# Kernel optimization log

Hardware: AMD Instinct MI355X
Metric: run time of the kernel (lower is better)

## Reference

```python
import jax, jax.numpy as jnp
import numpy as np

KH = KW = 3
STRIDE = 1
PAD = 1
DIL = 1


def _bilinear_sample(img, py, px):
    Hin, Win = img.shape[-2], img.shape[-1]
    y0 = jnp.floor(py)
    x0 = jnp.floor(px)
    y0i = y0.astype(jnp.int32)
    x0i = x0.astype(jnp.int32)
    wy = py - y0
    wx = px - x0

    def get(yi, xi):
        valid = (yi >= 0) & (yi < Hin) & (xi >= 0) & (xi < Win)
        yc = jnp.clip(yi, 0, Hin - 1)
        xc = jnp.clip(xi, 0, Win - 1)
        v = img[:, yc, xc]  # [C, K, H, W]
        return v * valid[None].astype(img.dtype)

    v00 = get(y0i, x0i)
    v01 = get(y0i, x0i + 1)
    v10 = get(y0i + 1, x0i)
    v11 = get(y0i + 1, x0i + 1)
    return (v00 * (1 - wy) * (1 - wx) + v01 * (1 - wy) * wx
            + v10 * wy * (1 - wx) + v11 * wy * wx)  # [C, K, H, W]


def _deform_conv(input, offset, mask, weight, bias):
    B, C, H, W = input.shape
    outH = (H + 2 * PAD - DIL * (KH - 1) - 1) // STRIDE + 1
    outW = (W + 2 * PAD - DIL * (KW - 1) - 1) // STRIDE + 1
    K = KH * KW
    # NOTE: DepthOffset in the original source overwrites its computed
    # depth-guided offsets with zeros and detaches them, so the effective
    # sampling offset is just `offset` (standard modulated deform conv, DCNv2).
    off = offset.reshape(B, K, 2, outH, outW)
    off_y = off[:, :, 0]  # [B, K, outH, outW]
    off_x = off[:, :, 1]
    ky = (jnp.arange(K) // KW) * DIL  # kernel-tap row offsets
    kx = (jnp.arange(K) % KW) * DIL
    ys = jnp.arange(outH) * STRIDE - PAD
    xs = jnp.arange(outW) * STRIDE - PAD
    base_y = (ky[:, None, None] + ys[None, :, None]).astype(input.dtype)  # [K, outH, 1]
    base_x = (kx[:, None, None] + xs[None, None, :]).astype(input.dtype)  # [K, 1, outW]
    py = base_y[None] + off_y  # [B, K, outH, outW]
    px = base_x[None] + off_x
    cols = jax.vmap(_bilinear_sample)(input, py, px)  # [B, C, K, outH, outW]
    cols = cols * mask[:, None]  # modulate by mask [B, 1, K, outH, outW]
    out = jnp.einsum('bckhw,ock->bohw', cols, weight.reshape(weight.shape[0], C, K))
    return out + bias[None, :, None, None]


def setup_inputs() -> dict:
    key = jax.random.key(0)
    ks = jax.random.split(key, 6)
    B, C, H, W = 4, 64, 128, 128
    O = 64
    fan_in = C * KH * KW
    bound = 1.0 / np.sqrt(fan_in)
    return {
        'input': jax.random.normal(ks[0], (B, C, H, W), dtype=jnp.float32),
        'depth': jax.random.uniform(ks[1], (B, 1, H, W), dtype=jnp.float32),
        'offset': jax.random.normal(ks[2], (B, 18, H, W), dtype=jnp.float32),
        'mask': jax.random.uniform(ks[3], (B, 9, H, W), dtype=jnp.float32),
        'weight': jax.random.uniform(ks[4], (O, C, KH, KW), dtype=jnp.float32,
                                     minval=-bound, maxval=bound),
        'bias': jax.random.uniform(ks[5], (O,), dtype=jnp.float32,
                                   minval=-bound, maxval=bound),
    }


def reference(input, depth, offset, mask, weight, bias):
    # depth-guided offsets are computed then zeroed+detached in the original
    # module, so depth does not influence the output.
    return _deform_conv(input, offset, mask, weight, bias)
```

## Files before the change

kernel.cpp:

```cpp
#include <hip/hip_runtime.h>


typedef __attribute__((ext_vector_type(8))) short bf16x8;
typedef __attribute__((ext_vector_type(4))) float f32x4;
typedef __attribute__((ext_vector_type(4))) unsigned int u32x4;

#define HH 128
#define WW 128
#define CC 64
#define OO 64
#define HW (128 * 128)

__device__ __forceinline__ unsigned f32_to_bf16_rne(float f) {
    unsigned u = __float_as_uint(f);
    return (u + 0x7FFFu + ((u >> 16) & 1u)) >> 16;
}

__global__ __launch_bounds__(256)
void prep_nhwc(const float* __restrict__ input,
               unsigned short* __restrict__ nhwc)
{
    __shared__ unsigned tile[64][33];
    const int tid = threadIdx.x;
    const int blk = blockIdx.x;
    const int b  = blk >> 9;
    const int y  = (blk >> 2) & 127;
    const int xbase = (blk & 3) * 32;
    #pragma unroll
    for (int it = 0; it < 8; ++it) {
        int flat = it * 256 + tid;
        int c = flat >> 5, x = flat & 31;
        float v = input[((b * 64 + c) * 128 + y) * 128 + xbase + x];
        tile[c][x] = f32_to_bf16_rne(v);
    }
    __syncthreads();
    {
        int x = tid >> 3, cg = tid & 7;
        unsigned r0 = tile[cg * 8 + 0][x], r1 = tile[cg * 8 + 1][x];
        unsigned r2 = tile[cg * 8 + 2][x], r3 = tile[cg * 8 + 3][x];
        unsigned r4 = tile[cg * 8 + 4][x], r5 = tile[cg * 8 + 5][x];
        unsigned r6 = tile[cg * 8 + 6][x], r7 = tile[cg * 8 + 7][x];
        u32x4 pk;
        pk[0] = r0 | (r1 << 16); pk[1] = r2 | (r3 << 16);
        pk[2] = r4 | (r5 << 16); pk[3] = r6 | (r7 << 16);
        *(u32x4*)(nhwc + ((size_t)((b * 128 + y) * 128 + xbase + x)) * 64 + cg * 8) = pk;
    }
}

__global__ __launch_bounds__(256)
void prep_w(const float* __restrict__ weight,
            unsigned short* __restrict__ wT2)
{
    const int d  = blockIdx.x * 256 + threadIdx.x;
    const int o  = d & 63;
    const int k8 = d >> 6;
    const int kt = k8 >> 3;
    const int c8 = k8 & 7;
    u32x4 pk;
    #pragma unroll
    for (int jj = 0; jj < 4; ++jj) {
        unsigned lo = f32_to_bf16_rne(weight[o * 576 + (c8 * 8 + 2 * jj)     * 9 + kt]);
        unsigned hi = f32_to_bf16_rne(weight[o * 576 + (c8 * 8 + 2 * jj + 1) * 9 + kt]);
        pk[jj] = lo | (hi << 16);
    }
    *(u32x4*)(wT2 + (size_t)d * 8) = pk;
}

__global__ __launch_bounds__(512)
void ddc_main(const unsigned short* __restrict__ nhwc,
              const unsigned short* __restrict__ wT2,
              const float* __restrict__ offset,
              const float* __restrict__ mask,
              const float* __restrict__ bias,
              float* __restrict__ out)
{
    __shared__ u32x4 wbuf[2560];

    const int blk  = blockIdx.x;
    const int b    = blk >> 7;
    const int h    = blk & 127;
    const int tid  = threadIdx.x;
    const int wave = tid >> 6;
    const int lane = tid & 63;
    const int l15  = lane & 15;
    const int kq   = lane >> 4;
    const int wpix = wave * 16 + l15;

    f32x4 acc[4];
    #pragma unroll
    for (int mt = 0; mt < 4; ++mt) acc[mt] = (f32x4){0.f, 0.f, 0.f, 0.f};

    const unsigned short* nb = nhwc + (size_t)b * HW * CC;
    const u32x4* wsrc = (const u32x4*)wT2;

    auto do_tap = [&](int kt, int ktl) {
        const float oy = offset[((b * 18 + 2 * kt)     * 128 + h) * 128 + wpix];
        const float ox = offset[((b * 18 + 2 * kt + 1) * 128 + h) * 128 + wpix];
        const float m  = mask  [((b * 9  + kt)         * 128 + h) * 128 + wpix];
        const float py = (float)(h - 1 + kt / 3) + oy;
        const float px = (float)(wpix - 1 + kt % 3) + ox;
        const float y0f = floorf(py), x0f = floorf(px);
        const int y0 = (int)y0f, x0 = (int)x0f;
        const float wy = py - y0f, wx = px - x0f;
        const int y1 = y0 + 1, x1 = x0 + 1;
        const bool vy0 = (y0 >= 0) & (y0 < HH);
        const bool vy1 = (y1 >= 0) & (y1 < HH);
        const bool vx0 = (x0 >= 0) & (x0 < WW);
        const bool vx1 = (x1 >= 0) & (x1 < WW);
        const int y0c = min(max(y0, 0), HH - 1), y1c = min(max(y1, 0), HH - 1);
        const int x0c = min(max(x0, 0), WW - 1), x1c = min(max(x1, 0), WW - 1);
        const float wy1 = 1.f - wy, wx1 = 1.f - wx;
        const float c00 = (vy0 && vx0) ? wy1 * wx1 * m : 0.f;
        const float c01 = (vy0 && vx1) ? wy1 * wx  * m : 0.f;
        const float c10 = (vy1 && vx0) ? wy  * wx1 * m : 0.f;
        const float c11 = (vy1 && vx1) ? wy  * wx  * m : 0.f;

        #pragma unroll
        for (int ks = 0; ks < 2; ++ks) {
            const int c0 = ks * 32 + kq * 8;

            const u32x4 w00 = *(const u32x4*)(nb + (y0c * WW + x0c) * CC + c0);
            const u32x4 w01 = *(const u32x4*)(nb + (y0c * WW + x1c) * CC + c0);
            const u32x4 w10 = *(const u32x4*)(nb + (y1c * WW + x0c) * CC + c0);
            const u32x4 w11 = *(const u32x4*)(nb + (y1c * WW + x1c) * CC + c0);

            u32x4 pk;
            #pragma unroll
            for (int j = 0; j < 4; ++j) {
                const float a0 = __uint_as_float(w00[j] << 16);
                const float a1 = __uint_as_float(w00[j] & 0xFFFF0000u);
                const float b0 = __uint_as_float(w01[j] << 16);
                const float b1 = __uint_as_float(w01[j] & 0xFFFF0000u);
                const float d0 = __uint_as_float(w10[j] << 16);
                const float d1 = __uint_as_float(w10[j] & 0xFFFF0000u);
                const float e0 = __uint_as_float(w11[j] << 16);
                const float e1 = __uint_as_float(w11[j] & 0xFFFF0000u);
                const float s0 = c00 * a0 + c01 * b0 + c10 * d0 + c11 * e0;
                const float s1 = c00 * a1 + c01 * b1 + c10 * d1 + c11 * e1;
                pk[j] = f32_to_bf16_rne(s0) | (f32_to_bf16_rne(s1) << 16);
            }
            const bf16x8 bfrag = __builtin_bit_cast(bf16x8, pk);

            #pragma unroll
            for (int mt = 0; mt < 4; ++mt) {
                const bf16x8 afrag = __builtin_bit_cast(bf16x8,
                    wbuf[(ktl * 8 + ks * 4 + kq) * 64 + mt * 16 + l15]);
                acc[mt] = __builtin_amdgcn_mfma_f32_16x16x32_bf16(afrag, bfrag, acc[mt], 0, 0, 0);
            }
        }
    };

    #pragma unroll
    for (int i = 0; i < 5; ++i) wbuf[i * 512 + tid] = wsrc[i * 512 + tid];
    __syncthreads();
    #pragma unroll
    for (int kt = 0; kt < 5; ++kt) do_tap(kt, kt);
    __syncthreads();

    #pragma unroll
    for (int i = 0; i < 4; ++i) wbuf[i * 512 + tid] = wsrc[2560 + i * 512 + tid];
    __syncthreads();
    #pragma unroll
    for (int kt = 5; kt < 9; ++kt) do_tap(kt, kt - 5);

    #pragma unroll
    for (int mt = 0; mt < 4; ++mt) {
        const f32x4 bv = *(const f32x4*)(bias + mt * 16 + kq * 4);
        #pragma unroll
        for (int r = 0; r < 4; ++r) {
            const int o = mt * 16 + kq * 4 + r;
            out[((b * 64 + o) * 128 + h) * 128 + wpix] = acc[mt][r] + bv[r];
        }
    }
}

extern "C" void kernel_launch(void* const* d_in, const int* in_sizes, int n_in,
                              void* d_out, int out_size, void* d_ws, size_t ws_size,
                              hipStream_t stream)
{
    const float* input  = (const float*)d_in[0];
    const float* offset = (const float*)d_in[2];
    const float* mask   = (const float*)d_in[3];
    const float* weight = (const float*)d_in[4];
    const float* bias   = (const float*)d_in[5];
    float* out = (float*)d_out;

    unsigned short* nhwc = (unsigned short*)d_ws;
    unsigned short* wT2  = nhwc + (size_t)4 * HW * CC;

    prep_nhwc<<<dim3(2048), dim3(256), 0, stream>>>(input, nhwc);
    prep_w<<<dim3(18), dim3(256), 0, stream>>>(weight, wT2);
    ddc_main<<<dim3(512), dim3(512), 0, stream>>>(nhwc, wT2, offset, mask, bias, out);
}
```

Baseline: 119.0 us.

## Stage an 8-row input window in LDS and double-buffer per-tap weights

The main kernel now loads an 8-row NHWC window around the output row into LDS, with an XOR swizzle on channel groups, so bilinear gathers read from LDS. Samples whose rows fall outside the window still read global memory. Weights are streamed one tap at a time through a double buffer instead of two large batches. The block index is remapped across batches, and the two prep kernels are merged into one launch. LDS use rises to roughly 144KB per block, which limits occupancy to one block per CU and adds a full 8-row window load before any compute starts.

Result: faster. 114.8 us (-3.5%).

```diff
diff --git a/kernel.cpp b/kernel.cpp
--- a/kernel.cpp
+++ b/kernel.cpp
@@ -17,12 +17,32 @@
 }
 
 __global__ __launch_bounds__(256)
-void prep_nhwc(const float* __restrict__ input,
-               unsigned short* __restrict__ nhwc)
+void prep_fused9(const float* __restrict__ input,
+                 unsigned short* __restrict__ nhwc,
+                 const float* __restrict__ weight,
+                 unsigned short* __restrict__ wT2)
 {
     __shared__ unsigned tile[64][33];
     const int tid = threadIdx.x;
     const int blk = blockIdx.x;
+
+    if (blk >= 2048) {
+        const int d  = (blk - 2048) * 256 + tid;
+        const int o  = d & 63;
+        const int k8 = d >> 6;
+        const int kt = k8 >> 3;
+        const int c8 = k8 & 7;
+        u32x4 pk;
+        #pragma unroll
+        for (int jj = 0; jj < 4; ++jj) {
+            unsigned lo = f32_to_bf16_rne(weight[o * 576 + (c8 * 8 + 2 * jj)     * 9 + kt]);
+            unsigned hi = f32_to_bf16_rne(weight[o * 576 + (c8 * 8 + 2 * jj + 1) * 9 + kt]);
+            pk[jj] = lo | (hi << 16);
+        }
+        *(u32x4*)(wT2 + (size_t)d * 8) = pk;
+        return;
+    }
+
     const int b  = blk >> 9;
     const int y  = (blk >> 2) & 127;
     const int xbase = (blk & 3) * 32;
@@ -47,36 +67,19 @@
     }
 }
 
-__global__ __launch_bounds__(256)
-void prep_w(const float* __restrict__ weight,
-            unsigned short* __restrict__ wT2)
-{
-    const int d  = blockIdx.x * 256 + threadIdx.x;
-    const int o  = d & 63;
-    const int k8 = d >> 6;
-    const int kt = k8 >> 3;
-    const int c8 = k8 & 7;
-    u32x4 pk;
-    #pragma unroll
-    for (int jj = 0; jj < 4; ++jj) {
-        unsigned lo = f32_to_bf16_rne(weight[o * 576 + (c8 * 8 + 2 * jj)     * 9 + kt]);
-        unsigned hi = f32_to_bf16_rne(weight[o * 576 + (c8 * 8 + 2 * jj + 1) * 9 + kt]);
-        pk[jj] = lo | (hi << 16);
-    }
-    *(u32x4*)(wT2 + (size_t)d * 8) = pk;
-}
-
 __global__ __launch_bounds__(512)
-void ddc_main(const unsigned short* __restrict__ nhwc,
+void ddc_win9(const unsigned short* __restrict__ nhwc,
               const unsigned short* __restrict__ wT2,
               const float* __restrict__ offset,
               const float* __restrict__ mask,
               const float* __restrict__ bias,
               float* __restrict__ out)
 {
-    __shared__ u32x4 wbuf[2560];
-
-    const int blk  = blockIdx.x;
+    __shared__ u32x4 win[8192];
+    __shared__ u32x4 wtap[2][512];
+
+    const int blk0 = blockIdx.x;
+    const int blk  = (blk0 & 7) * 64 + (blk0 >> 3);
     const int b    = blk >> 7;
     const int h    = blk & 127;
     const int tid  = threadIdx.x;
@@ -93,7 +96,22 @@
     const unsigned short* nb = nhwc + (size_t)b * HW * CC;
     const u32x4* wsrc = (const u32x4*)wT2;
 
-    auto do_tap = [&](int kt, int ktl) {
+    #pragma unroll
+    for (int i = 0; i < 16; ++i) {
+        const int slot = i >> 1;
+        const int y = h - 3 + slot;
+        if (y >= 0 && y < HH) {
+            const int q  = ((i & 1) << 9) + tid;
+            const int x  = q >> 3;
+            const int c8 = q & 7;
+            win[slot * 1024 + q] =
+                *(const u32x4*)(nb + ((size_t)(y * WW + x)) * CC + ((c8 ^ (x & 7)) << 3));
+        }
+    }
+    wtap[0][tid] = wsrc[tid];
+    __syncthreads();
+
+    auto do_tap = [&](int kt, const u32x4* __restrict__ wt) {
         const float oy = offset[((b * 18 + 2 * kt)     * 128 + h) * 128 + wpix];
         const float ox = offset[((b * 18 + 2 * kt + 1) * 128 + h) * 128 + wpix];
         const float m  = mask  [((b * 9  + kt)         * 128 + h) * 128 + wpix];
@@ -115,14 +133,30 @@
         const float c10 = (vy1 && vx0) ? wy  * wx1 * m : 0.f;
         const float c11 = (vy1 && vx1) ? wy  * wx  * m : 0.f;
 
+        const int s0 = y0c - (h - 3), s1 = y1c - (h - 3);
+        const bool in0 = ((unsigned)s0 < 8u);
+        const bool in1 = ((unsigned)s1 < 8u);
+        const int r0 = (in0 ? s0 : 0) * 1024;
+        const int r1 = (in1 ? s1 : 0) * 1024;
+        const int bx0 = x0c * 8, sx0 = x0c & 7;
+        const int bx1 = x1c * 8, sx1 = x1c & 7;
+
         #pragma unroll
         for (int ks = 0; ks < 2; ++ks) {
-            const int c0 = ks * 32 + kq * 8;
-
-            const u32x4 w00 = *(const u32x4*)(nb + (y0c * WW + x0c) * CC + c0);
-            const u32x4 w01 = *(const u32x4*)(nb + (y0c * WW + x1c) * CC + c0);
-            const u32x4 w10 = *(const u32x4*)(nb + (y1c * WW + x0c) * CC + c0);
-            const u32x4 w11 = *(const u32x4*)(nb + (y1c * WW + x1c) * CC + c0);
+            const int ch = ks * 4 + kq;
+
+            u32x4 w00 = win[r0 + bx0 + (ch ^ sx0)];
+            u32x4 w01 = win[r0 + bx1 + (ch ^ sx1)];
+            u32x4 w10 = win[r1 + bx0 + (ch ^ sx0)];
+            u32x4 w11 = win[r1 + bx1 + (ch ^ sx1)];
+            if (!in0) {
+                w00 = *(const u32x4*)(nb + ((size_t)y0c * WW + x0c) * CC + ch * 8);
+                w01 = *(const u32x4*)(nb + ((size_t)y0c * WW + x1c) * CC + ch * 8);
+            }
+            if (!in1) {
+                w10 = *(const u32x4*)(nb + ((size_t)y1c * WW + x0c) * CC + ch * 8);
+                w11 = *(const u32x4*)(nb + ((size_t)y1c * WW + x1c) * CC + ch * 8);
+            }
 
             u32x4 pk;
             #pragma unroll
@@ -135,33 +169,27 @@
                 const float d1 = __uint_as_float(w10[j] & 0xFFFF0000u);
                 const float e0 = __uint_as_float(w11[j] << 16);
                 const float e1 = __uint_as_float(w11[j] & 0xFFFF0000u);
-                const float s0 = c00 * a0 + c01 * b0 + c10 * d0 + c11 * e0;
-                const float s1 = c00 * a1 + c01 * b1 + c10 * d1 + c11 * e1;
-                pk[j] = f32_to_bf16_rne(s0) | (f32_to_bf16_rne(s1) << 16);
+                const float s0f = c00 * a0 + c01 * b0 + c10 * d0 + c11 * e0;
+                const float s1f = c00 * a1 + c01 * b1 + c10 * d1 + c11 * e1;
+                pk[j] = f32_to_bf16_rne(s0f) | (f32_to_bf16_rne(s1f) << 16);
             }
             const bf16x8 bfrag = __builtin_bit_cast(bf16x8, pk);
 
             #pragma unroll
             for (int mt = 0; mt < 4; ++mt) {
                 const bf16x8 afrag = __builtin_bit_cast(bf16x8,
-                    wbuf[(ktl * 8 + ks * 4 + kq) * 64 + mt * 16 + l15]);
+                    wt[(ks * 4 + kq) * 64 + mt * 16 + l15]);
                 acc[mt] = __builtin_amdgcn_mfma_f32_16x16x32_bf16(afrag, bfrag, acc[mt], 0, 0, 0);
             }
         }
     };
 
     #pragma unroll
-    for (int i = 0; i < 5; ++i) wbuf[i * 512 + tid] = wsrc[i * 512 + tid];
-    __syncthreads();
-    #pragma unroll
-    for (int kt = 0; kt < 5; ++kt) do_tap(kt, kt);
-    __syncthreads();
-
-    #pragma unroll
-    for (int i = 0; i < 4; ++i) wbuf[i * 512 + tid] = wsrc[2560 + i * 512 + tid];
-    __syncthreads();
-    #pragma unroll
-    for (int kt = 5; kt < 9; ++kt) do_tap(kt, kt - 5);
+    for (int kt = 0; kt < 9; ++kt) {
+        if (kt + 1 < 9) wtap[(kt + 1) & 1][tid] = wsrc[(kt + 1) * 512 + tid];
+        do_tap(kt, &wtap[kt & 1][0]);
+        __syncthreads();
+    }
 
     #pragma unroll
     for (int mt = 0; mt < 4; ++mt) {
@@ -188,7 +216,6 @@
     unsigned short* nhwc = (unsigned short*)d_ws;
     unsigned short* wT2  = nhwc + (size_t)4 * HW * CC;
 
-    prep_nhwc<<<dim3(2048), dim3(256), 0, stream>>>(input, nhwc);
-    prep_w<<<dim3(18), dim3(256), 0, stream>>>(weight, wT2);
-    ddc_main<<<dim3(512), dim3(512), 0, stream>>>(nhwc, wT2, offset, mask, bias, out);
-}
+    prep_fused9<<<dim3(2066), dim3(256), 0, stream>>>(input, nhwc, weight, wT2);
+    ddc_win9<<<dim3(512), dim3(512), 0, stream>>>(nhwc, wT2, offset, mask, bias, out);
+}
```
